# Kernel tuning notes

Hardware: AMD Instinct MI355X
Metric: run time of the kernel (lower is better)

## Reference

```python
import jax, jax.numpy as jnp
import numpy as np
import math

C = 256
GROUPS = 8
EPS = 1e-5


def setup_inputs() -> dict:
    key = jax.random.key(0)
    ks = jax.random.split(key, 12)
    b, c, h, w = 4, C, 64, 64
    s = 1.0 / math.sqrt(c)
    return {
        "x": jax.random.normal(ks[0], (b, c, h, w), dtype=jnp.float32),
        "gamma": jax.random.normal(ks[1], (c,), dtype=jnp.float32) * 0.1 + 1.0,
        "beta": jax.random.normal(ks[2], (c,), dtype=jnp.float32) * 0.1,
        "wq": jax.random.normal(ks[3], (c, c), dtype=jnp.float32) * s,
        "bq": jnp.zeros((c,), dtype=jnp.float32),
        "wk": jax.random.normal(ks[4], (c, c), dtype=jnp.float32) * s,
        "bk": jnp.zeros((c,), dtype=jnp.float32),
        "wv": jax.random.normal(ks[5], (c, c), dtype=jnp.float32) * s,
        "bv": jnp.zeros((c,), dtype=jnp.float32),
        "wp": jax.random.normal(ks[6], (c, c), dtype=jnp.float32) * s,
        "bp": jnp.zeros((c,), dtype=jnp.float32),
    }


def _group_norm(x, gamma, beta):
    b, c, h, w = x.shape
    xg = x.reshape(b, GROUPS, c // GROUPS, h * w)
    mean = xg.mean(axis=(2, 3), keepdims=True)
    var = xg.var(axis=(2, 3), keepdims=True)
    xn = ((xg - mean) * jax.lax.rsqrt(var + EPS)).reshape(b, c, h, w)
    return xn * gamma[None, :, None, None] + beta[None, :, None, None]


def _conv1x1(x, w, b):
    # 1x1 conv == per-pixel channel GEMM
    return jnp.einsum('oc,bchw->bohw', w, x) + b[None, :, None, None]


def reference(x, gamma, beta, wq, bq, wk, bk, wv, bv, wp, bp):
    b, c, h, w = x.shape
    n = h * w
    xn = _group_norm(x, gamma, beta)
    q = _conv1x1(xn, wq, bq).reshape(b, c, n)  # [b,c,n]
    k = _conv1x1(xn, wk, bk).reshape(b, c, n)
    v = _conv1x1(xn, wv, bv).reshape(b, c, n)
    scale = 1.0 / math.sqrt(c)
    scores = jnp.einsum('bcn,bcm->bnm', q, k) * scale  # [b,n,n]
    attn = jax.nn.softmax(scores, axis=-1)
    out = jnp.einsum('bnm,bcm->bcn', attn, v).reshape(b, c, h, w)
    return _conv1x1(out, wp, bp) + x
```

## Files before the change

### kernel.cpp

```cpp
#include <hip/hip_runtime.h>
#include <hip/hip_bf16.h>
#include <math.h>


#define CCH 256
#define NPIX 4096
#define NB 4
#define NG 8
#define EPS 1e-5f
#define NCHUNK 4

typedef __attribute__((ext_vector_type(8))) short short8;
typedef __attribute__((ext_vector_type(4))) short short4v;
typedef __attribute__((ext_vector_type(4))) float f32x4;
typedef __attribute__((ext_vector_type(16))) float f32x16;
typedef unsigned short ushort_t;
typedef unsigned char u8;

#define GLD16(g, l) __builtin_amdgcn_global_load_lds( \
    (const __attribute__((address_space(1))) unsigned int*)(g), \
    (__attribute__((address_space(3))) unsigned int*)(l), 16, 0, 0)

#define WAITV(n) asm volatile("s_waitcnt vmcnt(" #n ")" ::: "memory")

__device__ inline ushort_t f2bf(float x) {
    union { float f; unsigned u; } c; c.f = x;
    unsigned r = c.u + 0x7FFFu + ((c.u >> 16) & 1u);
    return (ushort_t)(r >> 16);
}
__device__ inline float bf2f(ushort_t h) {
    union { unsigned u; float f; } c; c.u = ((unsigned)h) << 16;
    return c.f;
}
__device__ inline u8 f2fp8(float x) {
    return (u8)(__builtin_amdgcn_cvt_pk_fp8_f32(x, x, 0, false) & 0xff);
}
__device__ inline long mk64(unsigned lo, unsigned hi) {
    return (long)(((unsigned long long)hi << 32) | lo);
}

__global__ __launch_bounds__(256) void gn1w(const float* __restrict__ x,
                                            const float* __restrict__ wq,
                                            const float* __restrict__ wk,
                                            const float* __restrict__ wv,
                                            const float* __restrict__ wp,
                                            float* __restrict__ part,
                                            ushort_t* __restrict__ wbf,
                                            ushort_t* __restrict__ wpbf) {
    int bid = blockIdx.x;
    int t = threadIdx.x;
    if (bid >= 256) {
        int widx = bid - 256;
        int wi = widx >> 6;
        const float* src = wi == 0 ? wq : wi == 1 ? wk : wi == 2 ? wv : wp;
        ushort_t* dst = wi == 3 ? wpbf : wbf + wi * 65536;
        int i = (widx & 63) * 1024 + t * 4;
        float4 v = *(const float4*)(src + i);
        short4v o;
        o[0] = (short)f2bf(v.x); o[1] = (short)f2bf(v.y);
        o[2] = (short)f2bf(v.z); o[3] = (short)f2bf(v.w);
        *(short4v*)(dst + i) = o;
        return;
    }
    int bg = bid >> 3;
    int slice = bid & 7;
    const float* base = x + (size_t)bg * 32 * NPIX + (size_t)slice * 16384;
    float s = 0.f, sq = 0.f;
    for (int i = t; i < 4096; i += 256) {
        float4 v = ((const float4*)base)[i];
        s  += v.x + v.y + v.z + v.w;
        sq += v.x*v.x + v.y*v.y + v.z*v.z + v.w*v.w;
    }
    for (int off = 32; off; off >>= 1) {
        s  += __shfl_down(s,  off);
        sq += __shfl_down(sq, off);
    }
    __shared__ float red[8];
    int wid = t >> 6;
    if ((t & 63) == 0) { red[wid*2] = s; red[wid*2+1] = sq; }
    __syncthreads();
    if (t == 0) {
        float ts = 0.f, tq = 0.f;
        for (int wv2 = 0; wv2 < 4; wv2++) { ts += red[wv2*2]; tq += red[wv2*2+1]; }
        part[bid*2] = ts; part[bid*2+1] = tq;
    }
}

__global__ __launch_bounds__(256) void gn_transpose(const float* __restrict__ x,
                                                    const float* __restrict__ part,
                                                    const float* __restrict__ gamma,
                                                    const float* __restrict__ beta,
                                                    ushort_t* __restrict__ xnT) {
    __shared__ float T[64][69];
    __shared__ float gmean[2], grstd[2];
    int t = threadIdx.x;
    int nBase = blockIdx.x * 64;
    int cBase = blockIdx.y * 64;
    int b = blockIdx.z;
    if (t < 2) {
        int g = (cBase >> 5) + t;
        float s = 0.f, sq = 0.f;
        for (int i = 0; i < 8; i++) {
            s  += part[((b*NG + g)*8 + i)*2];
            sq += part[((b*NG + g)*8 + i)*2 + 1];
        }
        const float inv = 1.f / 131072.f;
        float mean = s * inv;
        float var = sq * inv - mean * mean;
        gmean[t] = mean;
        grstd[t] = rsqrtf(var + EPS);
    }
    __syncthreads();
    const float* xb = x + (size_t)b * CCH * NPIX;
    int n4  = (t & 15) * 4;
    int cc0 = (t >> 4) * 4;
    for (int i = 0; i < 4; i++) {
        int cc = cc0 + i;
        int c = cBase + cc;
        int gi = cc >> 5;
        float ga = gamma[c] * grstd[gi];
        float be = beta[c] - gmean[gi] * ga;
        float4 v = *(const float4*)&xb[(size_t)c * NPIX + nBase + n4];
        T[cc][n4+0] = v.x * ga + be;
        T[cc][n4+1] = v.y * ga + be;
        T[cc][n4+2] = v.z * ga + be;
        T[cc][n4+3] = v.w * ga + be;
    }
    __syncthreads();
    int nn  = t >> 2;
    int ci0 = (t & 3) * 16;
    short8 o0, o1;
    for (int j = 0; j < 8; j++) {
        o0[j] = (short)f2bf(T[ci0 + j][nn]);
        o1[j] = (short)f2bf(T[ci0 + 8 + j][nn]);
    }
    ushort_t* dst = xnT + ((size_t)b * NPIX + nBase + nn) * CCH + cBase + ci0;
    *(short8*)dst = o0;
    *((short8*)dst + 1) = o1;
}

__global__ __launch_bounds__(256, 2) void qkv3(const ushort_t* __restrict__ xnT,
                                               const ushort_t* __restrict__ wbf,
                                               const float* __restrict__ bq,
                                               const float* __restrict__ bk,
                                               const float* __restrict__ bv,
                                               u8* __restrict__ qT,
                                               u8* __restrict__ kT,
                                               u8* __restrict__ vv) {
    __shared__ __align__(16) ushort_t As[2][4096];
    __shared__ __align__(16) ushort_t Bs[2][4096];
    int t = threadIdx.x;
    int w = t >> 6, l = t & 63, quad = l >> 4, l16 = l & 15;
    int z = blockIdx.z;
    const ushort_t* A; const ushort_t* B; int mBase, nBase;
    if (z < 2) { A = xnT; B = wbf + z * 65536; mBase = blockIdx.x * 128; nBase = blockIdx.y * 128; }
    else       { A = wbf + 131072; B = xnT;    mBase = blockIdx.y * 128; nBase = blockIdx.x * 128; }
    int m0 = (w & 1) * 64, n0 = (w >> 1) * 64;

    const f32x4 fz = {0.f, 0.f, 0.f, 0.f};
    f32x4 acc[4][4];
    #pragma unroll
    for (int i = 0; i < 4; i++)
        #pragma unroll
        for (int j = 0; j < 4; j++) acc[i][j] = fz;

    int srow = t >> 2;
    int slc  = (t & 3) ^ ((t >> 2) & 3);
    int sldso = (t >> 6) * 512;

    #pragma unroll
    for (int j = 0; j < 2; j++) {
        int row = 64*j + srow;
        GLD16(A + (size_t)(mBase + row) * 256 + slc * 8, &As[0][j*2048 + sldso]);
        GLD16(B + (size_t)(nBase + row) * 256 + slc * 8, &Bs[0][j*2048 + sldso]);
    }
    int buf = 0;
    for (int kb = 0; kb < 8; kb++) {
        __syncthreads();
        if (kb < 7) {
            #pragma unroll
            for (int j = 0; j < 2; j++) {
                int row = 64*j + srow;
                GLD16(A + (size_t)(mBase + row) * 256 + (kb+1)*32 + slc * 8, &As[buf^1][j*2048 + sldso]);
                GLD16(B + (size_t)(nBase + row) * 256 + (kb+1)*32 + slc * 8, &Bs[buf^1][j*2048 + sldso]);
            }
        }
        short8 af[4], bfr[4];
        #pragma unroll
        for (int mb = 0; mb < 4; mb++)
            af[mb] = *(short8*)&As[buf][(m0 + mb*16 + l16)*32 + ((quad ^ (l16 & 3)) * 8)];
        #pragma unroll
        for (int nb = 0; nb < 4; nb++)
            bfr[nb] = *(short8*)&Bs[buf][(n0 + nb*16 + l16)*32 + ((quad ^ (l16 & 3)) * 8)];
        #pragma unroll
        for (int mb = 0; mb < 4; mb++)
            #pragma unroll
            for (int nb = 0; nb < 4; nb++)
                acc[mb][nb] = __builtin_amdgcn_mfma_f32_16x16x32_bf16(af[mb], bfr[nb], acc[mb][nb], 0, 0, 0);
        buf ^= 1;
    }
    if (z < 2) {
        const float* bias = z ? bk : bq;
        u8* C = z ? kT : qT;
        #pragma unroll
        for (int nb = 0; nb < 4; nb++) {
            int n = nBase + n0 + nb*16 + l16;
            float bb = bias[n];
            #pragma unroll
            for (int mb = 0; mb < 4; mb++)
                #pragma unroll
                for (int r = 0; r < 4; r++) {
                    int m = mBase + m0 + mb*16 + quad*4 + r;
                    int nc = z ? (n ^ (((m >> 3) & 1) << 3)) : n;
                    C[(size_t)m * 256 + nc] = f2fp8(acc[mb][nb][r] + bb);
                }
        }
    } else {
        #pragma unroll
        for (int mb = 0; mb < 4; mb++)
            #pragma unroll
            for (int r = 0; r < 4; r++) {
                int m = mBase + m0 + mb*16 + quad*4 + r;
                float bb = bv[m];
                int sw8 = ((m >> 3) & 1) << 3;
                #pragma unroll
                for (int nb = 0; nb < 4; nb++) {
                    int n = nBase + n0 + nb*16 + l16;
                    vv[((size_t)(n >> 12) * 256 + m) * 4096 + ((n & 4095) ^ sw8)] = f2fp8(acc[mb][nb][r] + bb);
                }
            }
    }
}

__global__ __launch_bounds__(256, 2) void flash_attn(const u8* __restrict__ qT,
                                                     const u8* __restrict__ kT,
                                                     const u8* __restrict__ vv,
                                                     ushort_t* __restrict__ Op0,
                                                     ushort_t* __restrict__ Op1,
                                                     ushort_t* __restrict__ Op2,
                                                     ushort_t* __restrict__ Op3,
                                                     float* __restrict__ lsum) {
    __shared__ __align__(16) u8 KsAll[3 * 8192];
    __shared__ __align__(16) u8 VsAll[3 * 8192];
    int t = threadIdx.x;
    int w = t >> 6, l = t & 63;
    int l32 = l & 31, hl = l >> 5;
    int flat = blockIdx.x;
    int xcd = flat & 7;
    int ix = flat >> 3;
    int combo = xcd + 8 * (ix >> 5);
    int qg = ix & 31;
    int chunk = combo & 3, b = combo >> 2;
    int qw = qg * 128 + w * 32;

    long qf[16];
    {
        const u8* qrow = qT + ((size_t)b * NPIX + qw + l32) * 256 + hl * 8;
        #pragma unroll
        for (int cb = 0; cb < 16; cb++) qf[cb] = *(const long*)(qrow + cb * 16);
    }

    f32x16 accO[8];
    #pragma unroll
    for (int i = 0; i < 8; i++)
        #pragma unroll
        for (int r = 0; r < 16; r++) accO[i][r] = 0.f;
    float lqa = 0.f;

    const u8* kbase = kT + (size_t)b * NPIX * 256;
    const u8* vbase = vv + (size_t)b * 256 * NPIX;

    const float SC = 0.0625f * 1.44269504089f;
    int mStart = chunk * (NPIX / NCHUNK);
    const int NT = (NPIX / NCHUNK) / 32;

    const u8* kaddr[2];
    const u8* vaddr[2];
    #pragma unroll
    for (int j = 0; j < 2; j++) {
        int n = j * 256 + t;
        int kkv = n >> 4, kcb = (n & 15) ^ (kkv & 7);
        int vc = n >> 1,  vsw = (n & 1) ^ ((vc >> 2) & 1);
        kaddr[j] = kbase + (size_t)(mStart + kkv) * 256 + kcb * 16;
        vaddr[j] = vbase + (size_t)vc * NPIX + mStart + vsw * 16;
    }

    int g8 = (hl ^ ((l32 >> 3) & 1)) * 8;
    int kO[8];
    #pragma unroll
    for (int c = 0; c < 8; c++) kO[c] = l32 * 256 + ((c ^ (l32 & 7)) * 16) + g8;
    int sw0 = (l32 >> 2) & 1;
    int vO0 = l32 * 32 + (sw0 ^ 0) * 16 + g8;
    int vO1 = l32 * 32 + (sw0 ^ 1) * 16 + g8;

#define LDK(c) (*(const long*)&KsAll[kO[(c) & 7] + (((c) & 8) << 4)])
#define LDV0(m) (*(const long*)&VsAll[vO0 + (m) * 1024])
#define LDV1(m) (*(const long*)&VsAll[vO1 + (m) * 1024])

#define KISSUE(tile, slot) { \
        unsigned koff_ = (unsigned)(tile) * 8192u; \
        _Pragma("unroll") \
        for (int j = 0; j < 2; j++) \
            GLD16(kaddr[j] + koff_, &KsAll[(slot)*8192 + (j*256 + t)*16]); }
#define VISSUE(tile, slot) { \
        unsigned voff_ = (unsigned)(tile) * 32u; \
        _Pragma("unroll") \
        for (int j = 0; j < 2; j++) \
            GLD16(vaddr[j] + voff_, &VsAll[(slot)*8192 + (j*256 + t)*16]); }

#define SOFTMAX_PACK() { \
        float p_[16]; float q0_ = 0.f, q1_ = 0.f; \
        _Pragma("unroll") \
        for (int r = 0; r < 16; r++) { \
            float pe_ = exp2f(fmaf(sTa[r], SC, -5.0f)); \
            pe_ = fminf(pe_, 240.f); \
            p_[r] = pe_; \
            if (r & 1) q1_ += pe_; else q0_ += pe_; \
        } \
        lqa += q0_ + q1_; \
        unsigned pk0_ = (unsigned)__builtin_amdgcn_cvt_pk_fp8_f32(p_[2], p_[3], \
                        __builtin_amdgcn_cvt_pk_fp8_f32(p_[0], p_[1], 0, false), true); \
        unsigned pk1_ = (unsigned)__builtin_amdgcn_cvt_pk_fp8_f32(p_[6], p_[7], \
                        __builtin_amdgcn_cvt_pk_fp8_f32(p_[4], p_[5], 0, false), true); \
        unsigned pk2_ = (unsigned)__builtin_amdgcn_cvt_pk_fp8_f32(p_[10], p_[11], \
                        __builtin_amdgcn_cvt_pk_fp8_f32(p_[8], p_[9], 0, false), true); \
        unsigned pk3_ = (unsigned)__builtin_amdgcn_cvt_pk_fp8_f32(p_[14], p_[15], \
                        __builtin_amdgcn_cvt_pk_fp8_f32(p_[12], p_[13], 0, false), true); \
        asm("v_permlane32_swap_b32 %0, %1" : "+v"(pk0_), "+v"(pk1_)); \
        asm("v_permlane32_swap_b32 %0, %1" : "+v"(pk2_), "+v"(pk3_)); \
        B0 = mk64(pk0_, pk1_); \
        B1 = mk64(pk2_, pk3_); }

#define BURST() { \
        _Pragma("unroll") \
        for (int r = 0; r < 16; r++) sTa[r] = 0.f; \
        _Pragma("unroll") \
        for (int m = 0; m < 8; m++) { \
            sTa = __builtin_amdgcn_mfma_f32_32x32x16_fp8_fp8(LDK(2*m), qf[2*m], sTa, 0, 0, 0); \
            accO[m] = __builtin_amdgcn_mfma_f32_32x32x16_fp8_fp8(LDV0(m), B0, accO[m], 0, 0, 0); \
            sTa = __builtin_amdgcn_mfma_f32_32x32x16_fp8_fp8(LDK(2*m+1), qf[2*m+1], sTa, 0, 0, 0); \
            accO[m] = __builtin_amdgcn_mfma_f32_32x32x16_fp8_fp8(LDV1(m), B1, accO[m], 0, 0, 0); \
        } }

    KISSUE(0, 0);
    VISSUE(0, 0);
    KISSUE(1, 1);
    WAITV(4);
    __builtin_amdgcn_s_barrier();

    f32x16 sTa;
    #pragma unroll
    for (int r = 0; r < 16; r++) sTa[r] = 0.f;
    #pragma unroll
    for (int cb = 0; cb < 16; cb++)
        sTa = __builtin_amdgcn_mfma_f32_32x32x16_fp8_fp8(LDK(cb), qf[cb], sTa, 0, 0, 0);
    long B0, B1;
    SOFTMAX_PACK();

    #pragma unroll
    for (int c = 0; c < 8; c++) kO[c] += 8192;

    int ks_r = 1, ks_w = 2, vs_r = 0, vs_w = 1;
    #pragma unroll 1
    for (int tt = 0; tt < NT - 2; ++tt) {
        KISSUE(tt + 2, ks_w);
        VISSUE(tt + 1, vs_w);
        WAITV(4);
        __builtin_amdgcn_s_barrier();
        __builtin_amdgcn_sched_barrier(0);
        __builtin_amdgcn_s_setprio(1);
        BURST();
        __builtin_amdgcn_s_setprio(0);
        SOFTMAX_PACK();
        int dK = (ks_r == 2) ? -16384 : 8192;
        int dV = (vs_r == 2) ? -16384 : 8192;
        #pragma unroll
        for (int c = 0; c < 8; c++) kO[c] += dK;
        vO0 += dV; vO1 += dV;
        ks_r = ks_r + 1; if (ks_r == 3) ks_r = 0;
        ks_w = ks_w + 1; if (ks_w == 3) ks_w = 0;
        vs_r = vs_r + 1; if (vs_r == 3) vs_r = 0;
        vs_w = vs_w + 1; if (vs_w == 3) vs_w = 0;
    }

    VISSUE(NT - 1, vs_w);
    WAITV(2);
    __builtin_amdgcn_s_barrier();
    __builtin_amdgcn_sched_barrier(0);
    __builtin_amdgcn_s_setprio(1);
    BURST();
    __builtin_amdgcn_s_setprio(0);
    SOFTMAX_PACK();
    {
        int dV = (vs_r == 2) ? -16384 : 8192;
        vO0 += dV; vO1 += dV;
        vs_r = vs_r + 1; if (vs_r == 3) vs_r = 0;
    }

    WAITV(0);
    __builtin_amdgcn_s_barrier();
    {
        __builtin_amdgcn_s_setprio(1);
        #pragma unroll
        for (int m = 0; m < 8; m++) {
            accO[m] = __builtin_amdgcn_mfma_f32_32x32x16_fp8_fp8(LDV0(m), B0, accO[m], 0, 0, 0);
            accO[m] = __builtin_amdgcn_mfma_f32_32x32x16_fp8_fp8(LDV1(m), B1, accO[m], 0, 0, 0);
        }
        __builtin_amdgcn_s_setprio(0);
    }

    {
        float v = lqa + __shfl_xor(lqa, 32);
        if (hl == 0)
            lsum[((size_t)chunk * NB + b) * NPIX + qw + l32] = v;
    }
    ushort_t* op = chunk == 0 ? Op0 : chunk == 1 ? Op1 : chunk == 2 ? Op2 : Op3;
    size_t rowb = ((size_t)b * NPIX + qw + l32) * CCH;
    #pragma unroll
    for (int cblk = 0; cblk < 8; cblk++)
        #pragma unroll
        for (int a = 0; a < 4; a++) {
            short4v o;
            #pragma unroll
            for (int r = 0; r < 4; r++) o[r] = (short)f2bf(accO[cblk][a*4 + r]);
            *(short4v*)&op[rowb + cblk*32 + a*8 + hl*4] = o;
        }
#undef LDK
#undef LDV0
#undef LDV1
#undef KISSUE
#undef VISSUE
#undef SOFTMAX_PACK
#undef BURST
}

__global__ __launch_bounds__(256) void attn_combine(ushort_t* __restrict__ Op0,
                                                    const ushort_t* __restrict__ Op1,
                                                    const ushort_t* __restrict__ Op2,
                                                    const ushort_t* __restrict__ Op3,
                                                    const float* __restrict__ lsum) {
    const size_t BN = (size_t)NB * NPIX;
    size_t base = ((size_t)blockIdx.x * 256 + threadIdx.x) * 4;
    size_t bn = base >> 8;
    float li = 1.f / (lsum[bn] + lsum[BN + bn] + lsum[2*BN + bn] + lsum[3*BN + bn]);
    short4v a0 = *(short4v*)&Op0[base];
    short4v a1 = *(const short4v*)&Op1[base];
    short4v a2 = *(const short4v*)&Op2[base];
    short4v a3 = *(const short4v*)&Op3[base];
    short4v o;
    #pragma unroll
    for (int i = 0; i < 4; i++) {
        float v = (bf2f((ushort_t)a0[i]) + bf2f((ushort_t)a1[i]) +
                   bf2f((ushort_t)a2[i]) + bf2f((ushort_t)a3[i])) * li;
        o[i] = (short)f2bf(v);
    }
    *(short4v*)&Op0[base] = o;
}

__global__ __launch_bounds__(256, 2) void projk(const ushort_t* __restrict__ wpbf,
                                                const ushort_t* __restrict__ aoT,
                                                const float* __restrict__ bp,
                                                const float* __restrict__ x,
                                                float* __restrict__ out) {
    __shared__ __align__(16) ushort_t As[2][4096];
    __shared__ __align__(16) ushort_t Bs[2][4096];
    int t = threadIdx.x;
    int w = t >> 6, l = t & 63, quad = l >> 4, l16 = l & 15;
    int mBase = blockIdx.y * 128, nBase = blockIdx.x * 128;
    int m0 = (w & 1) * 64, n0 = (w >> 1) * 64;

    const f32x4 fz = {0.f, 0.f, 0.f, 0.f};
    f32x4 acc[4][4];
    #pragma unroll
    for (int i = 0; i < 4; i++)
        #pragma unroll
        for (int j = 0; j < 4; j++) acc[i][j] = fz;

    int srow = t >> 2;
    int slc  = (t & 3) ^ ((t >> 2) & 3);
    int sldso = (t >> 6) * 512;

    #pragma unroll
    for (int j = 0; j < 2; j++) {
        int row = 64*j + srow;
        GLD16(wpbf + (size_t)(mBase + row) * 256 + slc * 8, &As[0][j*2048 + sldso]);
        GLD16(aoT  + (size_t)(nBase + row) * 256 + slc * 8, &Bs[0][j*2048 + sldso]);
    }
    int buf = 0;
    for (int kb = 0; kb < 8; kb++) {
        __syncthreads();
        if (kb < 7) {
            #pragma unroll
            for (int j = 0; j < 2; j++) {
                int row = 64*j + srow;
                GLD16(wpbf + (size_t)(mBase + row) * 256 + (kb+1)*32 + slc * 8, &As[buf^1][j*2048 + sldso]);
                GLD16(aoT  + (size_t)(nBase + row) * 256 + (kb+1)*32 + slc * 8, &Bs[buf^1][j*2048 + sldso]);
            }
        }
        short8 af[4], bfr[4];
        #pragma unroll
        for (int mb = 0; mb < 4; mb++)
            af[mb] = *(short8*)&As[buf][(m0 + mb*16 + l16)*32 + ((quad ^ (l16 & 3)) * 8)];
        #pragma unroll
        for (int nb = 0; nb < 4; nb++)
            bfr[nb] = *(short8*)&Bs[buf][(n0 + nb*16 + l16)*32 + ((quad ^ (l16 & 3)) * 8)];
        #pragma unroll
        for (int mb = 0; mb < 4; mb++)
            #pragma unroll
            for (int nb = 0; nb < 4; nb++)
                acc[mb][nb] = __builtin_amdgcn_mfma_f32_16x16x32_bf16(af[mb], bfr[nb], acc[mb][nb], 0, 0, 0);
        buf ^= 1;
    }
    #pragma unroll
    for (int mb = 0; mb < 4; mb++)
        #pragma unroll
        for (int r = 0; r < 4; r++) {
            int m = mBase + m0 + mb*16 + quad*4 + r;
            float bb = bp[m];
            #pragma unroll
            for (int nb = 0; nb < 4; nb++) {
                int n = nBase + n0 + nb*16 + l16;
                size_t idx = ((size_t)(n >> 12) * 256 + m) * 4096 + (n & 4095);
                out[idx] = acc[mb][nb][r] + bb + x[idx];
            }
        }
}

extern "C" void kernel_launch(void* const* d_in, const int* in_sizes, int n_in,
                              void* d_out, int out_size, void* d_ws, size_t ws_size,
                              hipStream_t stream) {
    const float* x     = (const float*)d_in[0];
    const float* gamma = (const float*)d_in[1];
    const float* beta  = (const float*)d_in[2];
    const float* wq    = (const float*)d_in[3];
    const float* bq    = (const float*)d_in[4];
    const float* wk    = (const float*)d_in[5];
    const float* bk    = (const float*)d_in[6];
    const float* wv    = (const float*)d_in[7];
    const float* bv    = (const float*)d_in[8];
    const float* wp    = (const float*)d_in[9];
    const float* bp    = (const float*)d_in[10];
    float* out = (float*)d_out;

    const size_t SZ = (size_t)NB * NPIX * CCH;
    float* part  = (float*)d_ws;
    float* lsum  = part + 512;
    ushort_t* wpbf = (ushort_t*)(lsum + (size_t)NCHUNK * NB * NPIX);
    ushort_t* slot0 = wpbf + 65536;
    ushort_t* Op3 = slot0;
    u8* qT8 = (u8*)(slot0 + SZ);
    u8* kT8 = (u8*)(slot0 + 2*SZ);
    u8* vv8 = (u8*)(slot0 + 3*SZ);
    ushort_t* aoT = slot0 + 4*SZ;
    ushort_t* xnT = (ushort_t*)d_out;
    ushort_t* Op1 = (ushort_t*)d_out;
    ushort_t* Op2 = (ushort_t*)d_out + SZ;
    ushort_t* wbf = (ushort_t*)d_out + SZ;

    gn1w<<<512, 256, 0, stream>>>(x, wq, wk, wv, wp, part, wbf, wpbf);
    gn_transpose<<<dim3(64, 4, 4), 256, 0, stream>>>(x, part, gamma, beta, xnT);
    qkv3<<<dim3(128, 2, 3), 256, 0, stream>>>(xnT, wbf, bq, bk, bv, qT8, kT8, vv8);
    flash_attn<<<dim3(512), 256, 0, stream>>>(qT8, kT8, vv8, aoT, Op1, Op2, Op3, lsum);
    attn_combine<<<(int)(SZ / 1024), 256, 0, stream>>>(aoT, Op1, Op2, Op3, lsum);
    projk<<<dim3(128, 2), 256, 0, stream>>>(wpbf, aoT, bp, x, out);
}
```

Measured before the change: 195.9 us.

## Use 4-slot K/V LDS ring and sync once per two tiles in flash attention

Changes the flash attention K/V shared-memory ring from 3 to 4 slots. The main loop is unrolled to process two tiles per iteration, with a single vmcnt wait and barrier per pair and four global-to-LDS loads issued at once. The aim is to halve the barrier count and expose more load latency to overlap with MFMA work. The cost is LDS growing from 48KB to 64KB per block, which can limit occupancy at 2 blocks per CU, and waiting on vmcnt(0) drains every outstanding load each iteration.

```diff
diff --git a/kernel.cpp b/kernel.cpp
--- a/kernel.cpp
+++ b/kernel.cpp
@@ -240,8 +240,8 @@
                                                      ushort_t* __restrict__ Op2,
                                                      ushort_t* __restrict__ Op3,
                                                      float* __restrict__ lsum) {
-    __shared__ __align__(16) u8 KsAll[3 * 8192];
-    __shared__ __align__(16) u8 VsAll[3 * 8192];
+    __shared__ __align__(16) u8 KsAll[4 * 8192];
+    __shared__ __align__(16) u8 VsAll[4 * 8192];
     int t = threadIdx.x;
     int w = t >> 6, l = t & 63;
     int l32 = l & 31, hl = l >> 5;
@@ -272,7 +272,6 @@
 
     const float SC = 0.0625f * 1.44269504089f;
     int mStart = chunk * (NPIX / NCHUNK);
-    const int NT = (NPIX / NCHUNK) / 32;
 
     const u8* kaddr[2];
     const u8* vaddr[2];
@@ -342,10 +341,19 @@
             accO[m] = __builtin_amdgcn_mfma_f32_32x32x16_fp8_fp8(LDV1(m), B1, accO[m], 0, 0, 0); \
         } }
 
+#define ADV_K() { int d_ = (ksl == 3) ? -24576 : 8192; \
+        _Pragma("unroll") \
+        for (int c = 0; c < 8; c++) kO[c] += d_; \
+        ksl = (ksl + 1) & 3; }
+#define ADV_V() { int d_ = (vsl == 3) ? -24576 : 8192; \
+        vO0 += d_; vO1 += d_; vsl = (vsl + 1) & 3; }
+
     KISSUE(0, 0);
+    KISSUE(1, 1);
+    KISSUE(2, 2);
     VISSUE(0, 0);
-    KISSUE(1, 1);
-    WAITV(4);
+    VISSUE(1, 1);
+    WAITV(0);
     __builtin_amdgcn_s_barrier();
 
     f32x16 sTa;
@@ -357,57 +365,63 @@
     long B0, B1;
     SOFTMAX_PACK();
 
-    #pragma unroll
-    for (int c = 0; c < 8; c++) kO[c] += 8192;
-
-    int ks_r = 1, ks_w = 2, vs_r = 0, vs_w = 1;
+    int ksl = 0, vsl = 0;
+    ADV_K();
+
     #pragma unroll 1
-    for (int tt = 0; tt < NT - 2; ++tt) {
-        KISSUE(tt + 2, ks_w);
-        VISSUE(tt + 1, vs_w);
-        WAITV(4);
+    for (int j = 0; j < 14; ++j) {
+        int a = 2 * j;
+        WAITV(0);
         __builtin_amdgcn_s_barrier();
         __builtin_amdgcn_sched_barrier(0);
+        KISSUE(a + 3, (a + 3) & 3);
+        KISSUE(a + 4, (a + 4) & 3);
+        VISSUE(a + 2, (a + 2) & 3);
+        VISSUE(a + 3, (a + 3) & 3);
         __builtin_amdgcn_s_setprio(1);
         BURST();
         __builtin_amdgcn_s_setprio(0);
         SOFTMAX_PACK();
-        int dK = (ks_r == 2) ? -16384 : 8192;
-        int dV = (vs_r == 2) ? -16384 : 8192;
-        #pragma unroll
-        for (int c = 0; c < 8; c++) kO[c] += dK;
-        vO0 += dV; vO1 += dV;
-        ks_r = ks_r + 1; if (ks_r == 3) ks_r = 0;
-        ks_w = ks_w + 1; if (ks_w == 3) ks_w = 0;
-        vs_r = vs_r + 1; if (vs_r == 3) vs_r = 0;
-        vs_w = vs_w + 1; if (vs_w == 3) vs_w = 0;
-    }
-
-    VISSUE(NT - 1, vs_w);
-    WAITV(2);
+        ADV_K(); ADV_V();
+        __builtin_amdgcn_s_setprio(1);
+        BURST();
+        __builtin_amdgcn_s_setprio(0);
+        SOFTMAX_PACK();
+        ADV_K(); ADV_V();
+    }
+
+    WAITV(0);
+    __builtin_amdgcn_s_barrier();
+    __builtin_amdgcn_sched_barrier(0);
+    KISSUE(31, 31 & 3);
+    VISSUE(30, 30 & 3);
+    VISSUE(31, 31 & 3);
+    __builtin_amdgcn_s_setprio(1);
+    BURST();
+    __builtin_amdgcn_s_setprio(0);
+    SOFTMAX_PACK();
+    ADV_K(); ADV_V();
+    __builtin_amdgcn_s_setprio(1);
+    BURST();
+    __builtin_amdgcn_s_setprio(0);
+    SOFTMAX_PACK();
+    ADV_K(); ADV_V();
+
+    WAITV(0);
     __builtin_amdgcn_s_barrier();
     __builtin_amdgcn_sched_barrier(0);
     __builtin_amdgcn_s_setprio(1);
     BURST();
     __builtin_amdgcn_s_setprio(0);
     SOFTMAX_PACK();
-    {
-        int dV = (vs_r == 2) ? -16384 : 8192;
-        vO0 += dV; vO1 += dV;
-        vs_r = vs_r + 1; if (vs_r == 3) vs_r = 0;
-    }
-
-    WAITV(0);
-    __builtin_amdgcn_s_barrier();
-    {
-        __builtin_amdgcn_s_setprio(1);
-        #pragma unroll
-        for (int m = 0; m < 8; m++) {
-            accO[m] = __builtin_amdgcn_mfma_f32_32x32x16_fp8_fp8(LDV0(m), B0, accO[m], 0, 0, 0);
-            accO[m] = __builtin_amdgcn_mfma_f32_32x32x16_fp8_fp8(LDV1(m), B1, accO[m], 0, 0, 0);
-        }
-        __builtin_amdgcn_s_setprio(0);
-    }
+    ADV_V();
+    __builtin_amdgcn_s_setprio(1);
+    #pragma unroll
+    for (int m = 0; m < 8; m++) {
+        accO[m] = __builtin_amdgcn_mfma_f32_32x32x16_fp8_fp8(LDV0(m), B0, accO[m], 0, 0, 0);
+        accO[m] = __builtin_amdgcn_mfma_f32_32x32x16_fp8_fp8(LDV1(m), B1, accO[m], 0, 0, 0);
+    }
+    __builtin_amdgcn_s_setprio(0);
 
     {
         float v = lqa + __shfl_xor(lqa, 32);
@@ -432,6 +446,8 @@
 #undef VISSUE
 #undef SOFTMAX_PACK
 #undef BURST
+#undef ADV_K
+#undef ADV_V
 }
 
 __global__ __launch_bounds__(256) void attn_combine(ushort_t* __restrict__ Op0,
```

New measurement: 200.2 us. 2.2% more time.
